# Optimization experiments

Measured on AMD Instinct MI355X. Metric: run time of the kernel, lower is better.

The kernel has to match this reference:

```python
import jax, jax.numpy as jnp
import numpy as np


def conv1x1(x, w, b):
    # x: [B,C,H,W], w: [O,C], b: [O]
    return jnp.einsum('oc,bchw->bohw', w, x) + b[None, :, None, None]


def interp_bilinear_ac(x, oh, ow):
    # bilinear resize with align_corners=True, x: [B,C,H,W] -> [B,C,oh,ow]
    B, C, H, W = x.shape
    if (H, W) == (oh, ow):
        return x
    ys = jnp.linspace(0.0, H - 1.0, oh)
    xs = jnp.linspace(0.0, W - 1.0, ow)
    y0 = jnp.clip(jnp.floor(ys).astype(jnp.int32), 0, H - 1)
    y1 = jnp.minimum(y0 + 1, H - 1)
    x0 = jnp.clip(jnp.floor(xs).astype(jnp.int32), 0, W - 1)
    x1 = jnp.minimum(x0 + 1, W - 1)
    wy = (ys - y0).astype(x.dtype)
    wx = (xs - x0).astype(x.dtype)
    top = x[:, :, y0, :] * (1 - wy)[None, None, :, None] + x[:, :, y1, :] * wy[None, None, :, None]
    out = top[:, :, :, x0] * (1 - wx)[None, None, None, :] + top[:, :, :, x1] * wx[None, None, None, :]
    return out


def non_local(x, qw, qb, kw, kb, vw, vb, ow_, ob):
    B, C, H, W = x.shape
    HW = H * W
    q = conv1x1(x, qw, qb).reshape(B, -1, HW)  # [B, Ci, HW]
    k = conv1x1(x, kw, kb).reshape(B, -1, HW)
    v = conv1x1(x, vw, vb).reshape(B, -1, HW)
    attn = jnp.einsum('bci,bcj->bij', q, k)     # [B, HW, HW]
    attn = jax.nn.softmax(attn, axis=-1)
    out = jnp.einsum('bcj,bij->bci', v, attn)   # [B, Ci, HW]
    out = out.reshape(B, -1, H, W)
    return conv1x1(out, ow_, ob)


def _forward(x1, x2, x3, x4, qw, qb, kw, kb, vw, vb, ow_, ob, g1w, g1b, g2w, g2b):
    H1, W1 = x1.shape[2], x1.shape[3]
    x2_up = interp_bilinear_ac(x2, H1, W1)
    x3_up = interp_bilinear_ac(x3, H1, W1)
    x4_up = interp_bilinear_ac(x4, H1, W1)
    gf = jnp.concatenate([x1, x2_up, x3_up, x4_up], axis=1)  # [B, 128, H1, W1]
    gf = non_local(gf, qw, qb, kw, kb, vw, vb, ow_, ob)
    h = jax.nn.relu(conv1x1(gf, g1w, g1b))
    sw = jax.nn.sigmoid(conv1x1(h, g2w, g2b))                # [B, 128, H1, W1]
    w1, w2, w3, w4 = sw[:, :32], sw[:, 32:64], sw[:, 64:96], sw[:, 96:128]
    x1_out = x1 * (1 + w1)
    x2_out = x2 * (1 + interp_bilinear_ac(w2, x2.shape[2], x2.shape[3]))
    x3_out = x3 * (1 + interp_bilinear_ac(w3, x3.shape[2], x3.shape[3]))
    x4_out = x4 * (1 + interp_bilinear_ac(w4, x4.shape[2], x4.shape[3]))
    return (x1_out, x2_out, x3_out, x4_out)


def setup_inputs() -> dict:
    key = jax.random.key(0)
    ks = jax.random.split(key, 16)
    C = 128  # channel*4
    Ci = 64  # inter_channel
    Cg = 32
    d = {
        'x1': jax.random.normal(ks[0], (8, 32, 64, 64), jnp.float32),
        'x2': jax.random.normal(ks[1], (8, 32, 32, 32), jnp.float32),
        'x3': jax.random.normal(ks[2], (8, 32, 16, 16), jnp.float32),
        'x4': jax.random.normal(ks[3], (8, 32, 8, 8), jnp.float32),
        'qw': jax.random.normal(ks[4], (Ci, C), jnp.float32) * 0.05,
        'qb': jnp.zeros((Ci,), jnp.float32),
        'kw': jax.random.normal(ks[5], (Ci, C), jnp.float32) * 0.05,
        'kb': jnp.zeros((Ci,), jnp.float32),
        'vw': jax.random.normal(ks[6], (Ci, C), jnp.float32) * 0.05,
        'vb': jnp.zeros((Ci,), jnp.float32),
        'ow_': jax.random.normal(ks[7], (C, Ci), jnp.float32) * 0.05,
        'ob': jnp.zeros((C,), jnp.float32),
        'g1w': jax.random.normal(ks[8], (Cg, C), jnp.float32) * 0.05,
        'g1b': jnp.zeros((Cg,), jnp.float32),
        'g2w': jax.random.normal(ks[9], (C, Cg), jnp.float32) * 0.05,
        'g2b': jnp.zeros((C,), jnp.float32),
    }
    return d


def reference(x1, x2, x3, x4, qw, qb, kw, kb, vw, vb, ow_, ob, g1w, g1b, g2w, g2b):
    return _forward(x1, x2, x3, x4, qw, qb, kw, kb, vw, vb, ow_, ob, g1w, g1b, g2w, g2b)
```

## Files before the change

### kernel.cpp

```cpp
#include <hip/hip_runtime.h>
#include <hip/hip_bf16.h>


typedef __attribute__((ext_vector_type(8))) short s16x8;
typedef __attribute__((ext_vector_type(4))) float f32x4;
typedef __attribute__((ext_vector_type(16))) float f32x16;

#define LOG2E 1.44269504088896340736f

__device__ __forceinline__ unsigned int f2bf(float f) {
    unsigned int u = __float_as_uint(f);
    u += 0x7fffu + ((u >> 16) & 1u);
    return u >> 16;
}
__device__ __forceinline__ unsigned int pk2bf(float a, float b) {
    union { __hip_bfloat162 h; unsigned int u; } cv;
    cv.h = __float22bfloat162_rn(make_float2(a, b));
    return cv.u;
}
__device__ __forceinline__ float bf2f(unsigned short u) {
    return __uint_as_float((unsigned int)u << 16);
}
__device__ __forceinline__ float fexp2(float x) { return __builtin_amdgcn_exp2f(x); }
__device__ __forceinline__ float frcp(float x)  { return __builtin_amdgcn_rcpf(x); }

__global__ __launch_bounds__(256) void k_prep(
    const float* __restrict__ qw, const float* __restrict__ qb,
    const float* __restrict__ kw, const float* __restrict__ kb,
    const float* __restrict__ vw, const float* __restrict__ vb,
    const float* __restrict__ ow, const float* __restrict__ g1w,
    const float* __restrict__ g2w,
    unsigned short* __restrict__ WTb, float* __restrict__ bqkv,
    unsigned short* __restrict__ owb, unsigned short* __restrict__ g1wb,
    unsigned short* __restrict__ g2wb) {
  int t = blockIdx.x * 256 + threadIdx.x;
  if (t < 192 * 128) {
    int oc = t >> 7, c = t & 127;
    float v;
    if (oc < 64)       v = qw[oc * 128 + c] * LOG2E;
    else if (oc < 128) v = kw[(oc - 64) * 128 + c];
    else               v = vw[(oc - 128) * 128 + c];
    WTb[t] = (unsigned short)f2bf(v);
  }
  if (t < 192) {
    float v;
    if (t < 64)       v = qb[t] * LOG2E;
    else if (t < 128) v = kb[t - 64];
    else              v = vb[t - 128];
    bqkv[t] = v;
  }
  if (t < 128 * 64) owb[t]  = (unsigned short)f2bf(ow[t]);
  if (t < 32 * 128) g1wb[t] = (unsigned short)f2bf(g1w[t]);
  if (t < 128 * 32) g2wb[t] = (unsigned short)f2bf(g2w[t]);
}

__global__ __launch_bounds__(256, 4) void k_qkv(
    const float* __restrict__ x1, const float* __restrict__ x2,
    const float* __restrict__ x3, const float* __restrict__ x4,
    const unsigned short* __restrict__ WTb, const float* __restrict__ bqkv,
    unsigned short* __restrict__ Qg, unsigned short* __restrict__ Kg,
    unsigned short* __restrict__ Vg) {
  __shared__ __align__(16) unsigned short gfb[32 * 136];
  unsigned int* gfbu = (unsigned int*)gfb;

  const int blk = blockIdx.x;
  const int b = blk >> 7;
  const int i0 = (blk & 127) << 5;
  const int t = threadIdx.x;
  const int wv = t >> 6, lane = t & 63;
  const int r = lane & 15, qd = lane >> 4;
  f32x4 zf = {0.f, 0.f, 0.f, 0.f};

  {
    const int cp = t >> 2, q = t & 3;
    const int c0 = cp << 1;
    const int pbase = q << 3;
    const int oy = i0 >> 6;
    const int ox0 = (i0 & 63) | (q << 3);

    if (cp < 16) {
      const float* s0 = x1 + (((b * 32 + c0) << 12) + (oy << 6) + ox0);
      const float* s1 = s0 + 4096;
      #pragma unroll
      for (int k4 = 0; k4 < 2; k4++) {
        float4 va = ((const float4*)s0)[k4];
        float4 vb = ((const float4*)s1)[k4];
        int p = pbase + k4 * 4;
        gfbu[(p + 0) * 68 + cp] = pk2bf(va.x, vb.x);
        gfbu[(p + 1) * 68 + cp] = pk2bf(va.y, vb.y);
        gfbu[(p + 2) * 68 + cp] = pk2bf(va.z, vb.z);
        gfbu[(p + 3) * 68 + cp] = pk2bf(va.w, vb.w);
      }
    } else {
      const float* base; int S, cs;
      if (cp < 32)      { base = x2; S = 32; cs = c0 - 32; }
      else if (cp < 48) { base = x3; S = 16; cs = c0 - 64; }
      else              { base = x4; S = 8;  cs = c0 - 96; }
      const float* pl0 = base + (b * 32 + cs) * S * S;
      const float* pl1 = pl0 + S * S;
      float yf = (float)oy * (float)(S - 1) * (1.0f / 63.0f);
      int y0 = (int)yf; if (y0 > S - 1) y0 = S - 1;
      int y1 = y0 + 1;  if (y1 > S - 1) y1 = S - 1;
      float wy = yf - (float)y0;
      const float* r00 = pl0 + y0 * S; const float* r01 = pl0 + y1 * S;
      const float* r10 = pl1 + y0 * S; const float* r11 = pl1 + y1 * S;
      for (int k = 0; k < 8; k++) {
        int ox = ox0 + k;
        float xf = (float)ox * (float)(S - 1) * (1.0f / 63.0f);
        int xx0 = (int)xf; if (xx0 > S - 1) xx0 = S - 1;
        int xx1 = xx0 + 1; if (xx1 > S - 1) xx1 = S - 1;
        float wx = xf - (float)xx0;
        float a0 = r00[xx0] + wx * (r00[xx1] - r00[xx0]);
        float b0 = r01[xx0] + wx * (r01[xx1] - r01[xx0]);
        float v0 = a0 + wy * (b0 - a0);
        float a1 = r10[xx0] + wx * (r10[xx1] - r10[xx0]);
        float b1 = r11[xx0] + wx * (r11[xx1] - r11[xx0]);
        float v1 = a1 + wy * (b1 - a1);
        gfbu[(pbase + k) * 68 + cp] = pk2bf(v0, v1);
      }
    }
  }
  __syncthreads();

  const int ocb = wv * 48;
  s16x8 af[3][4];
  float4 bias[3];
  #pragma unroll
  for (int mti = 0; mti < 3; mti++) {
    #pragma unroll
    for (int ks = 0; ks < 4; ks++)
      af[mti][ks] = *(const s16x8*)&WTb[(ocb + mti * 16 + r) * 128 + ks * 32 + qd * 8];
    bias[mti] = *(const float4*)&bqkv[ocb + mti * 16 + qd * 4];
  }

  #pragma unroll
  for (int nt = 0; nt < 2; nt++) {
    s16x8 bfr[4];
    #pragma unroll
    for (int ks = 0; ks < 4; ks++)
      bfr[ks] = *(const s16x8*)&gfb[(nt * 16 + r) * 136 + ks * 32 + qd * 8];
    f32x4 acc[3] = {zf, zf, zf};
    #pragma unroll
    for (int ks = 0; ks < 4; ks++)
      #pragma unroll
      for (int mti = 0; mti < 3; mti++)
        acc[mti] = __builtin_amdgcn_mfma_f32_16x16x32_bf16(af[mti][ks], bfr[ks], acc[mti], 0, 0, 0);

    const int pos = i0 + nt * 16 + r;
    #pragma unroll
    for (int mti = 0; mti < 3; mti++) {
      const int gmt = wv * 3 + mti;
      float ax = acc[mti].x + bias[mti].x;
      float ay = acc[mti].y + bias[mti].y;
      float az = acc[mti].z + bias[mti].z;
      float aw = acc[mti].w + bias[mti].w;
      if (gmt < 4) {
        uint2 w; w.x = pk2bf(ax, ay); w.y = pk2bf(az, aw);
        *(uint2*)&Qg[(((b << 12) + pos) << 6) + gmt * 16 + qd * 4] = w;
      } else if (gmt < 8) {
        uint2 w; w.x = pk2bf(ax, ay); w.y = pk2bf(az, aw);
        *(uint2*)&Kg[(((b << 12) + pos) << 6) + (gmt - 4) * 16 + qd * 4] = w;
      } else {
        int ocv = (gmt - 8) * 16 + qd * 4;
        Vg[((b * 64 + ocv + 0) << 12) + pos] = (unsigned short)f2bf(ax);
        Vg[((b * 64 + ocv + 1) << 12) + pos] = (unsigned short)f2bf(ay);
        Vg[((b * 64 + ocv + 2) << 12) + pos] = (unsigned short)f2bf(az);
        Vg[((b * 64 + ocv + 3) << 12) + pos] = (unsigned short)f2bf(aw);
      }
    }
  }
}

__global__ __launch_bounds__(256, 4) void k_attn(
    const unsigned short* __restrict__ Qg, const unsigned short* __restrict__ Kg,
    const unsigned short* __restrict__ Vg, unsigned short* __restrict__ Op,
    float* __restrict__ Lp) {
  __shared__ __align__(16) unsigned short Kl[2][64 * 72];
  __shared__ __align__(16) unsigned short Vl[2][64 * 72];

  const int b = blockIdx.x >> 7;
  const int part = (blockIdx.x >> 5) & 3;
  const int qg = blockIdx.x & 31;
  const int i0 = qg << 7;
  const int t = threadIdx.x;
  const int wv = t >> 6, lane = t & 63;
  const int q = lane & 31, hi = lane >> 5;
  const int qbase = i0 + wv * 32;

  s16x8 qf[4];
  #pragma unroll
  for (int kc = 0; kc < 4; kc++)
    qf[kc] = *(const s16x8*)&Qg[(((b << 12) + qbase + q) << 6) + kc * 16 + hi * 8];

  f32x16 acc[2];
  #pragma unroll
  for (int m = 0; m < 2; m++)
    #pragma unroll
    for (int e = 0; e < 16; e++) acc[m][e] = 0.f;
  float ls = 0.f;

  const int srow = t >> 3, sseg = t & 7;
  const unsigned short* kt0 = &Kg[(((b << 12) + (part << 10) + srow) << 6) + sseg * 8];
  const unsigned short* vt0 = &Vg[((b * 64 + srow) << 12) + (part << 10) + sseg * 8];
  uint4 pk0 = *(const uint4*)(kt0);
  uint4 pk1 = *(const uint4*)(kt0 + (32 << 6));
  uint4 pv0 = *(const uint4*)(vt0);
  uint4 pv1 = *(const uint4*)(vt0 + (32 << 12));

  for (int it = 0; it < 16; it++) {
    unsigned short* Kb = Kl[it & 1];
    unsigned short* Vb = Vl[it & 1];
    *(uint4*)&Kb[srow * 72 + sseg * 8] = pk0;
    *(uint4*)&Kb[(srow + 32) * 72 + sseg * 8] = pk1;
    *(uint4*)&Vb[srow * 72 + sseg * 8] = pv0;
    *(uint4*)&Vb[(srow + 32) * 72 + sseg * 8] = pv1;
    __syncthreads();
    if (it < 15) {
      int j0 = (it + 1) << 6;
      pk0 = *(const uint4*)(kt0 + (j0 << 6));
      pk1 = *(const uint4*)(kt0 + ((j0 + 32) << 6));
      pv0 = *(const uint4*)(vt0 + j0);
      pv1 = *(const uint4*)(vt0 + (32 << 12) + j0);
    }

    unsigned int pu[2][8];
    #pragma unroll
    for (int kt = 0; kt < 2; kt++) {
      f32x16 st;
      #pragma unroll
      for (int e = 0; e < 16; e++) st[e] = 0.f;
      #pragma unroll
      for (int kc = 0; kc < 4; kc++) {
        s16x8 kf = *(const s16x8*)&Kb[(kt * 32 + q) * 72 + kc * 16 + hi * 8];
        st = __builtin_amdgcn_mfma_f32_32x32x16_bf16(kf, qf[kc], st, 0, 0, 0);
      }
      float lsum = 0.f;
      #pragma unroll
      for (int i2 = 0; i2 < 8; i2++) {
        float p0 = fexp2(st[2 * i2]);
        float p1 = fexp2(st[2 * i2 + 1]);
        lsum += p0 + p1;
        pu[kt][i2] = pk2bf(p0, p1);
      }
      ls += lsum;
    }

    #pragma unroll
    for (int kt = 0; kt < 2; kt++) {
      #pragma unroll
      for (int c16 = 0; c16 < 2; c16++) {
        const int c16g = kt * 2 + c16;
        unsigned int a0 = pu[kt][c16 * 4 + 0], a1 = pu[kt][c16 * 4 + 1];
        unsigned int a2 = pu[kt][c16 * 4 + 2], a3 = pu[kt][c16 * 4 + 3];
        unsigned int k0 = hi ? a2 : a0, k1 = hi ? a3 : a1;
        unsigned int s0 = hi ? a0 : a2, s1 = hi ? a1 : a3;
        unsigned int r0 = __shfl_xor(s0, 32);
        unsigned int r1 = __shfl_xor(s1, 32);
        union { s16x8 v; unsigned int u[4]; } pb;
        pb.u[0] = hi ? r0 : k0;
        pb.u[1] = hi ? r1 : k1;
        pb.u[2] = hi ? k0 : r0;
        pb.u[3] = hi ? k1 : r1;
        #pragma unroll
        for (int mtv = 0; mtv < 2; mtv++) {
          s16x8 vf = *(const s16x8*)&Vb[(mtv * 32 + q) * 72 + c16g * 16 + hi * 8];
          acc[mtv] = __builtin_amdgcn_mfma_f32_32x32x16_bf16(vf, pb.v, acc[mtv], 0, 0, 0);
        }
      }
    }
  }

  ls += __shfl_xor(ls, 32);
  float inv = frcp(ls);
  const int qrow = qbase + q;
  unsigned short* orow = &Op[(((part * 8 + b) << 12) + qrow) << 6];
  #pragma unroll
  for (int mtv = 0; mtv < 2; mtv++) {
    #pragma unroll
    for (int i2 = 0; i2 < 8; i2++) {
      int dbase = ((2 * i2) & 3) + 8 * ((2 * i2) >> 2) + 4 * hi + mtv * 32;
      *(unsigned int*)&orow[dbase] =
          pk2bf(acc[mtv][2 * i2] * inv, acc[mtv][2 * i2 + 1] * inv);
    }
  }
  if (hi == 0) Lp[((part * 8 + b) << 12) + qrow] = ls;
}

__global__ __launch_bounds__(256, 4) void k_out(
    const unsigned short* __restrict__ Op, const float* __restrict__ Lp,
    const unsigned short* __restrict__ owb, const float* __restrict__ obias,
    const unsigned short* __restrict__ g1wb, const float* __restrict__ g1b,
    const unsigned short* __restrict__ g2wb, const float* __restrict__ g2b,
    const float* __restrict__ x1, float* __restrict__ out,
    unsigned short* __restrict__ SWb) {
  __shared__ __align__(16) unsigned short Ot[32 * 72];
  __shared__ __align__(16) unsigned short gf2t[32 * 136];
  __shared__ __align__(16) unsigned short ht[32 * 40];
  const int blk = blockIdx.x;
  const int b = blk >> 7;
  const int i0 = (blk & 127) << 5;
  const int t = threadIdx.x;
  const int wv = t >> 6, lane = t & 63;
  const int r = lane & 15, qd = lane >> 4;
  f32x4 zf = {0.f, 0.f, 0.f, 0.f};

  {
    const int pos = t >> 3, seg = t & 7;
    const int i = i0 + pos;
    float lp4[4], lsum = 0.f;
    #pragma unroll
    for (int p = 0; p < 4; p++) { lp4[p] = Lp[((p * 8 + b) << 12) + i]; lsum += lp4[p]; }
    float o[8];
    #pragma unroll
    for (int k = 0; k < 8; k++) o[k] = 0.f;
    float invs = frcp(lsum);
    #pragma unroll
    for (int p = 0; p < 4; p++) {
      float w = lp4[p] * invs;
      uint4 u = *(const uint4*)&Op[((((p * 8 + b) << 12) + i) << 6) + seg * 8];
      o[0] += w * __uint_as_float(u.x << 16);
      o[1] += w * __uint_as_float(u.x & 0xFFFF0000u);
      o[2] += w * __uint_as_float(u.y << 16);
      o[3] += w * __uint_as_float(u.y & 0xFFFF0000u);
      o[4] += w * __uint_as_float(u.z << 16);
      o[5] += w * __uint_as_float(u.z & 0xFFFF0000u);
      o[6] += w * __uint_as_float(u.w << 16);
      o[7] += w * __uint_as_float(u.w & 0xFFFF0000u);
    }
    unsigned int* dst = (unsigned int*)&Ot[pos * 72 + seg * 8];
    #pragma unroll
    for (int k = 0; k < 4; k++) dst[k] = pk2bf(o[2 * k], o[2 * k + 1]);
  }
  __syncthreads();

  {
    const int ocb = wv * 32;
    s16x8 af[2][2];
    #pragma unroll
    for (int mt = 0; mt < 2; mt++)
      #pragma unroll
      for (int ks = 0; ks < 2; ks++)
        af[mt][ks] = *(const s16x8*)&owb[(ocb + mt * 16 + r) * 64 + ks * 32 + qd * 8];
    float4 bias[2];
    #pragma unroll
    for (int mt = 0; mt < 2; mt++)
      bias[mt] = *(const float4*)&obias[ocb + mt * 16 + qd * 4];
    #pragma unroll
    for (int nt = 0; nt < 2; nt++) {
      s16x8 bfr[2];
      #pragma unroll
      for (int ks = 0; ks < 2; ks++)
        bfr[ks] = *(const s16x8*)&Ot[(nt * 16 + r) * 72 + ks * 32 + qd * 8];
      f32x4 acc[2] = {zf, zf};
      #pragma unroll
      for (int ks = 0; ks < 2; ks++)
        #pragma unroll
        for (int mt = 0; mt < 2; mt++)
          acc[mt] = __builtin_amdgcn_mfma_f32_16x16x32_bf16(af[mt][ks], bfr[ks], acc[mt], 0, 0, 0);
      #pragma unroll
      for (int mt = 0; mt < 2; mt++) {
        uint2 w;
        w.x = pk2bf(acc[mt].x + bias[mt].x, acc[mt].y + bias[mt].y);
        w.y = pk2bf(acc[mt].z + bias[mt].z, acc[mt].w + bias[mt].w);
        *(uint2*)&gf2t[(nt * 16 + r) * 136 + ocb + mt * 16 + qd * 4] = w;
      }
    }
  }
  __syncthreads();

  {
    const int mt = wv & 1, pt = wv >> 1;
    s16x8 af[4];
    #pragma unroll
    for (int ks = 0; ks < 4; ks++)
      af[ks] = *(const s16x8*)&g1wb[(mt * 16 + r) * 128 + ks * 32 + qd * 8];
    float4 bias = *(const float4*)&g1b[mt * 16 + qd * 4];
    s16x8 bfr[4];
    #pragma unroll
    for (int ks = 0; ks < 4; ks++)
      bfr[ks] = *(const s16x8*)&gf2t[(pt * 16 + r) * 136 + ks * 32 + qd * 8];
    f32x4 acc = zf;
    #pragma unroll
    for (int ks = 0; ks < 4; ks++)
      acc = __builtin_amdgcn_mfma_f32_16x16x32_bf16(af[ks], bfr[ks], acc, 0, 0, 0);
    uint2 w;
    w.x = pk2bf(fmaxf(acc.x + bias.x, 0.f), fmaxf(acc.y + bias.y, 0.f));
    w.y = pk2bf(fmaxf(acc.z + bias.z, 0.f), fmaxf(acc.w + bias.w, 0.f));
    *(uint2*)&ht[(pt * 16 + r) * 40 + mt * 16 + qd * 4] = w;
  }
  __syncthreads();

  {
    const int nb = wv * 32;
    s16x8 bfg[2];
    float bias[2];
    #pragma unroll
    for (int ntl = 0; ntl < 2; ntl++) {
      bfg[ntl] = *(const s16x8*)&g2wb[(nb + ntl * 16 + r) * 32 + qd * 8];
      bias[ntl] = g2b[nb + ntl * 16 + r];
    }
    #pragma unroll
    for (int mt = 0; mt < 2; mt++) {
      s16x8 af = *(const s16x8*)&ht[(mt * 16 + r) * 40 + qd * 8];
      #pragma unroll
      for (int ntl = 0; ntl < 2; ntl++) {
        f32x4 acc = __builtin_amdgcn_mfma_f32_16x16x32_bf16(af, bfg[ntl], zf, 0, 0, 0);
        const int oc3 = nb + ntl * 16 + r;
        float s0 = frcp(1.0f + fexp2(-LOG2E * (acc.x + bias[ntl])));
        float s1 = frcp(1.0f + fexp2(-LOG2E * (acc.y + bias[ntl])));
        float s2 = frcp(1.0f + fexp2(-LOG2E * (acc.z + bias[ntl])));
        float s3 = frcp(1.0f + fexp2(-LOG2E * (acc.w + bias[ntl])));
        if (nb == 0) {
          const int off = ((b * 32 + oc3) << 12) + i0 + mt * 16 + qd * 4;
          float4 xv = *(const float4*)&x1[off];
          float4 o4;
          o4.x = xv.x * (1.f + s0); o4.y = xv.y * (1.f + s1);
          o4.z = xv.z * (1.f + s2); o4.w = xv.w * (1.f + s3);
          *(float4*)&out[off] = o4;
        } else {
          uint2 w; w.x = pk2bf(s0, s1); w.y = pk2bf(s2, s3);
          *(uint2*)&SWb[((b * 128 + oc3) << 12) + i0 + mt * 16 + qd * 4] = w;
        }
      }
    }
  }
}

__device__ __forceinline__ float bilin64(const unsigned short* __restrict__ p,
                                         int oy, int ox, int n) {
  float yf = (float)oy * 63.0f / (float)n;
  int y0 = (int)yf; if (y0 > 63) y0 = 63;
  int y1 = y0 + 1;  if (y1 > 63) y1 = 63;
  float wy = yf - (float)y0;
  float xf = (float)ox * 63.0f / (float)n;
  int x0 = (int)xf; if (x0 > 63) x0 = 63;
  int x1 = x0 + 1;  if (x1 > 63) x1 = 63;
  float wx = xf - (float)x0;
  float v00 = bf2f(p[y0 * 64 + x0]), v01 = bf2f(p[y0 * 64 + x1]);
  float v10 = bf2f(p[y1 * 64 + x0]), v11 = bf2f(p[y1 * 64 + x1]);
  float top = v00 + wx * (v01 - v00);
  float bot = v10 + wx * (v11 - v10);
  return top + wy * (bot - top);
}

__global__ __launch_bounds__(256) void k_final(
    const float* __restrict__ x2, const float* __restrict__ x3,
    const float* __restrict__ x4,
    const unsigned short* __restrict__ SWb, float* __restrict__ out) {
  const int N1 = 1048576, N2 = 262144, N3 = 65536, N4 = 16384;
  int idx = blockIdx.x * 256 + threadIdx.x;
  if (idx < N2) {
    int b = idx >> 15, rr = idx & 32767;
    int c = rr >> 10, oy = (rr >> 5) & 31, ox = rr & 31;
    float w = bilin64(SWb + ((b * 128 + 32 + c) << 12), oy, ox, 31);
    out[N1 + idx] = x2[idx] * (1.f + w);
  } else if (idx < N2 + N3) {
    int i3 = idx - N2;
    int b = i3 >> 13, rr = i3 & 8191;
    int c = rr >> 8, oy = (rr >> 4) & 15, ox = rr & 15;
    float w = bilin64(SWb + ((b * 128 + 64 + c) << 12), oy, ox, 15);
    out[N1 + idx] = x3[i3] * (1.f + w);
  } else if (idx < N2 + N3 + N4) {
    int i4 = idx - N2 - N3;
    int b = i4 >> 11, rr = i4 & 2047;
    int c = rr >> 6, oy = (rr >> 3) & 7, ox = rr & 7;
    float w = bilin64(SWb + ((b * 128 + 96 + c) << 12), oy, ox, 7);
    out[N1 + idx] = x4[i4] * (1.f + w);
  }
}

extern "C" void kernel_launch(void* const* d_in, const int* in_sizes, int n_in,
                              void* d_out, int out_size, void* d_ws, size_t ws_size,
                              hipStream_t stream) {
  const float* x1  = (const float*)d_in[0];
  const float* x2  = (const float*)d_in[1];
  const float* x3  = (const float*)d_in[2];
  const float* x4  = (const float*)d_in[3];
  const float* qw  = (const float*)d_in[4];
  const float* qb  = (const float*)d_in[5];
  const float* kw  = (const float*)d_in[6];
  const float* kb  = (const float*)d_in[7];
  const float* vw  = (const float*)d_in[8];
  const float* vb  = (const float*)d_in[9];
  const float* ow  = (const float*)d_in[10];
  const float* ob  = (const float*)d_in[11];
  const float* g1w = (const float*)d_in[12];
  const float* g1b = (const float*)d_in[13];
  const float* g2w = (const float*)d_in[14];
  const float* g2b = (const float*)d_in[15];
  float* out = (float*)d_out;

  char* ws = (char*)d_ws;
  unsigned short* Qg  = (unsigned short*)(ws + 0);
  unsigned short* Kg  = (unsigned short*)(ws + 4194304);
  unsigned short* Vg  = (unsigned short*)(ws + 8388608);
  unsigned short* SWb = (unsigned short*)(ws + 0);
  unsigned short* Op  = (unsigned short*)(ws + 12582912);
  float* Lp   = (float*)(ws + 29360128);
  unsigned short* WTb = (unsigned short*)(ws + 29884416);
  float* bqkv = (float*)(ws + 29933568);
  unsigned short* owb  = (unsigned short*)(ws + 29934592);
  unsigned short* g1wb = (unsigned short*)(ws + 29950976);
  unsigned short* g2wb = (unsigned short*)(ws + 29959168);

  k_prep<<<96, 256, 0, stream>>>(qw, qb, kw, kb, vw, vb, ow, g1w, g2w,
                                 WTb, bqkv, owb, g1wb, g2wb);
  k_qkv<<<1024, 256, 0, stream>>>(x1, x2, x3, x4, WTb, bqkv, Qg, Kg, Vg);
  k_attn<<<1024, 256, 0, stream>>>(Qg, Kg, Vg, Op, Lp);
  k_out<<<1024, 256, 0, stream>>>(Op, Lp, owb, ob, g1wb, g1b, g2wb, g2b,
                                  x1, out, SWb);
  k_final<<<1344, 256, 0, stream>>>(x2, x3, x4, SWb, out);
}
```

Measured before the change: 173.8 us.

## Fuse output projection, gating and final resize into attention via atomic counters

Merges k_out and k_final into k_attn. The last of the four key-partition blocks for each query group, detected with an atomic counter, merges the partial results and runs the output conv and gating MLP. The last of those blocks per batch then does the bilinear resize and the final multiply. This removes two kernel launches and their inter-kernel gaps. In exchange, the tail work is serialized onto a few blocks, with one block per batch doing all the x2/x3/x4 output work, and a memset is added to reset the counters.

```diff
diff --git a/kernel.cpp b/kernel.cpp
--- a/kernel.cpp
+++ b/kernel.cpp
@@ -174,9 +174,17 @@
 __global__ __launch_bounds__(256, 4) void k_attn(
     const unsigned short* __restrict__ Qg, const unsigned short* __restrict__ Kg,
     const unsigned short* __restrict__ Vg, unsigned short* __restrict__ Op,
-    float* __restrict__ Lp) {
+    float* __restrict__ Lp,
+    const unsigned short* __restrict__ owb, const float* __restrict__ obias,
+    const unsigned short* __restrict__ g1wb, const float* __restrict__ g1b,
+    const unsigned short* __restrict__ g2wb, const float* __restrict__ g2b,
+    const float* __restrict__ x1, const float* __restrict__ x2,
+    const float* __restrict__ x3, const float* __restrict__ x4,
+    float* __restrict__ out, unsigned short* __restrict__ SWb2,
+    unsigned int* __restrict__ cnt1, unsigned int* __restrict__ cnt2) {
   __shared__ __align__(16) unsigned short Kl[2][64 * 72];
   __shared__ __align__(16) unsigned short Vl[2][64 * 72];
+  __shared__ unsigned int whoS;
 
   const int b = blockIdx.x >> 7;
   const int part = (blockIdx.x >> 5) & 3;
@@ -187,285 +195,313 @@
   const int q = lane & 31, hi = lane >> 5;
   const int qbase = i0 + wv * 32;
 
-  s16x8 qf[4];
-  #pragma unroll
-  for (int kc = 0; kc < 4; kc++)
-    qf[kc] = *(const s16x8*)&Qg[(((b << 12) + qbase + q) << 6) + kc * 16 + hi * 8];
-
-  f32x16 acc[2];
-  #pragma unroll
-  for (int m = 0; m < 2; m++)
-    #pragma unroll
-    for (int e = 0; e < 16; e++) acc[m][e] = 0.f;
-  float ls = 0.f;
-
-  const int srow = t >> 3, sseg = t & 7;
-  const unsigned short* kt0 = &Kg[(((b << 12) + (part << 10) + srow) << 6) + sseg * 8];
-  const unsigned short* vt0 = &Vg[((b * 64 + srow) << 12) + (part << 10) + sseg * 8];
-  uint4 pk0 = *(const uint4*)(kt0);
-  uint4 pk1 = *(const uint4*)(kt0 + (32 << 6));
-  uint4 pv0 = *(const uint4*)(vt0);
-  uint4 pv1 = *(const uint4*)(vt0 + (32 << 12));
-
-  for (int it = 0; it < 16; it++) {
-    unsigned short* Kb = Kl[it & 1];
-    unsigned short* Vb = Vl[it & 1];
-    *(uint4*)&Kb[srow * 72 + sseg * 8] = pk0;
-    *(uint4*)&Kb[(srow + 32) * 72 + sseg * 8] = pk1;
-    *(uint4*)&Vb[srow * 72 + sseg * 8] = pv0;
-    *(uint4*)&Vb[(srow + 32) * 72 + sseg * 8] = pv1;
-    __syncthreads();
-    if (it < 15) {
-      int j0 = (it + 1) << 6;
-      pk0 = *(const uint4*)(kt0 + (j0 << 6));
-      pk1 = *(const uint4*)(kt0 + ((j0 + 32) << 6));
-      pv0 = *(const uint4*)(vt0 + j0);
-      pv1 = *(const uint4*)(vt0 + (32 << 12) + j0);
-    }
-
-    unsigned int pu[2][8];
-    #pragma unroll
-    for (int kt = 0; kt < 2; kt++) {
-      f32x16 st;
-      #pragma unroll
-      for (int e = 0; e < 16; e++) st[e] = 0.f;
-      #pragma unroll
-      for (int kc = 0; kc < 4; kc++) {
-        s16x8 kf = *(const s16x8*)&Kb[(kt * 32 + q) * 72 + kc * 16 + hi * 8];
-        st = __builtin_amdgcn_mfma_f32_32x32x16_bf16(kf, qf[kc], st, 0, 0, 0);
-      }
-      float lsum = 0.f;
+  {
+    s16x8 qf[4];
+    #pragma unroll
+    for (int kc = 0; kc < 4; kc++)
+      qf[kc] = *(const s16x8*)&Qg[(((b << 12) + qbase + q) << 6) + kc * 16 + hi * 8];
+
+    f32x16 acc[2];
+    #pragma unroll
+    for (int m = 0; m < 2; m++)
+      #pragma unroll
+      for (int e = 0; e < 16; e++) acc[m][e] = 0.f;
+    float ls = 0.f;
+
+    const int srow = t >> 3, sseg = t & 7;
+    const unsigned short* kt0 = &Kg[(((b << 12) + (part << 10) + srow) << 6) + sseg * 8];
+    const unsigned short* vt0 = &Vg[((b * 64 + srow) << 12) + (part << 10) + sseg * 8];
+    uint4 pk0 = *(const uint4*)(kt0);
+    uint4 pk1 = *(const uint4*)(kt0 + (32 << 6));
+    uint4 pv0 = *(const uint4*)(vt0);
+    uint4 pv1 = *(const uint4*)(vt0 + (32 << 12));
+
+    for (int it = 0; it < 16; it++) {
+      unsigned short* Kb = Kl[it & 1];
+      unsigned short* Vb = Vl[it & 1];
+      *(uint4*)&Kb[srow * 72 + sseg * 8] = pk0;
+      *(uint4*)&Kb[(srow + 32) * 72 + sseg * 8] = pk1;
+      *(uint4*)&Vb[srow * 72 + sseg * 8] = pv0;
+      *(uint4*)&Vb[(srow + 32) * 72 + sseg * 8] = pv1;
+      __syncthreads();
+      if (it < 15) {
+        int j0 = (it + 1) << 6;
+        pk0 = *(const uint4*)(kt0 + (j0 << 6));
+        pk1 = *(const uint4*)(kt0 + ((j0 + 32) << 6));
+        pv0 = *(const uint4*)(vt0 + j0);
+        pv1 = *(const uint4*)(vt0 + (32 << 12) + j0);
+      }
+
+      unsigned int pu[2][8];
+      #pragma unroll
+      for (int kt = 0; kt < 2; kt++) {
+        f32x16 st;
+        #pragma unroll
+        for (int e = 0; e < 16; e++) st[e] = 0.f;
+        #pragma unroll
+        for (int kc = 0; kc < 4; kc++) {
+          s16x8 kf = *(const s16x8*)&Kb[(kt * 32 + q) * 72 + kc * 16 + hi * 8];
+          st = __builtin_amdgcn_mfma_f32_32x32x16_bf16(kf, qf[kc], st, 0, 0, 0);
+        }
+        float lsum = 0.f;
+        #pragma unroll
+        for (int i2 = 0; i2 < 8; i2++) {
+          float p0 = fexp2(st[2 * i2]);
+          float p1 = fexp2(st[2 * i2 + 1]);
+          lsum += p0 + p1;
+          pu[kt][i2] = pk2bf(p0, p1);
+        }
+        ls += lsum;
+      }
+
+      #pragma unroll
+      for (int kt = 0; kt < 2; kt++) {
+        #pragma unroll
+        for (int c16 = 0; c16 < 2; c16++) {
+          const int c16g = kt * 2 + c16;
+          unsigned int a0 = pu[kt][c16 * 4 + 0], a1 = pu[kt][c16 * 4 + 1];
+          unsigned int a2 = pu[kt][c16 * 4 + 2], a3 = pu[kt][c16 * 4 + 3];
+          unsigned int k0 = hi ? a2 : a0, k1 = hi ? a3 : a1;
+          unsigned int s0 = hi ? a0 : a2, s1 = hi ? a1 : a3;
+          unsigned int r0 = __shfl_xor(s0, 32);
+          unsigned int r1 = __shfl_xor(s1, 32);
+          union { s16x8 v; unsigned int u[4]; } pb;
+          pb.u[0] = hi ? r0 : k0;
+          pb.u[1] = hi ? r1 : k1;
+          pb.u[2] = hi ? k0 : r0;
+          pb.u[3] = hi ? k1 : r1;
+          #pragma unroll
+          for (int mtv = 0; mtv < 2; mtv++) {
+            s16x8 vf = *(const s16x8*)&Vl[it & 1][(mtv * 32 + q) * 72 + c16g * 16 + hi * 8];
+            acc[mtv] = __builtin_amdgcn_mfma_f32_32x32x16_bf16(vf, pb.v, acc[mtv], 0, 0, 0);
+          }
+        }
+      }
+    }
+
+    ls += __shfl_xor(ls, 32);
+    float inv = frcp(ls);
+    const int qrow = qbase + q;
+    unsigned short* orow = &Op[(((part * 8 + b) << 12) + qrow) << 6];
+    #pragma unroll
+    for (int mtv = 0; mtv < 2; mtv++) {
       #pragma unroll
       for (int i2 = 0; i2 < 8; i2++) {
-        float p0 = fexp2(st[2 * i2]);
-        float p1 = fexp2(st[2 * i2 + 1]);
-        lsum += p0 + p1;
-        pu[kt][i2] = pk2bf(p0, p1);
-      }
-      ls += lsum;
-    }
-
-    #pragma unroll
-    for (int kt = 0; kt < 2; kt++) {
-      #pragma unroll
-      for (int c16 = 0; c16 < 2; c16++) {
-        const int c16g = kt * 2 + c16;
-        unsigned int a0 = pu[kt][c16 * 4 + 0], a1 = pu[kt][c16 * 4 + 1];
-        unsigned int a2 = pu[kt][c16 * 4 + 2], a3 = pu[kt][c16 * 4 + 3];
-        unsigned int k0 = hi ? a2 : a0, k1 = hi ? a3 : a1;
-        unsigned int s0 = hi ? a0 : a2, s1 = hi ? a1 : a3;
-        unsigned int r0 = __shfl_xor(s0, 32);
-        unsigned int r1 = __shfl_xor(s1, 32);
-        union { s16x8 v; unsigned int u[4]; } pb;
-        pb.u[0] = hi ? r0 : k0;
-        pb.u[1] = hi ? r1 : k1;
-        pb.u[2] = hi ? k0 : r0;
-        pb.u[3] = hi ? k1 : r1;
-        #pragma unroll
-        for (int mtv = 0; mtv < 2; mtv++) {
-          s16x8 vf = *(const s16x8*)&Vb[(mtv * 32 + q) * 72 + c16g * 16 + hi * 8];
-          acc[mtv] = __builtin_amdgcn_mfma_f32_32x32x16_bf16(vf, pb.v, acc[mtv], 0, 0, 0);
-        }
-      }
-    }
-  }
-
-  ls += __shfl_xor(ls, 32);
-  float inv = frcp(ls);
-  const int qrow = qbase + q;
-  unsigned short* orow = &Op[(((part * 8 + b) << 12) + qrow) << 6];
-  #pragma unroll
-  for (int mtv = 0; mtv < 2; mtv++) {
-    #pragma unroll
-    for (int i2 = 0; i2 < 8; i2++) {
-      int dbase = ((2 * i2) & 3) + 8 * ((2 * i2) >> 2) + 4 * hi + mtv * 32;
-      *(unsigned int*)&orow[dbase] =
-          pk2bf(acc[mtv][2 * i2] * inv, acc[mtv][2 * i2 + 1] * inv);
-    }
-  }
-  if (hi == 0) Lp[((part * 8 + b) << 12) + qrow] = ls;
-}
-
-__global__ __launch_bounds__(256, 4) void k_out(
-    const unsigned short* __restrict__ Op, const float* __restrict__ Lp,
-    const unsigned short* __restrict__ owb, const float* __restrict__ obias,
-    const unsigned short* __restrict__ g1wb, const float* __restrict__ g1b,
-    const unsigned short* __restrict__ g2wb, const float* __restrict__ g2b,
-    const float* __restrict__ x1, float* __restrict__ out,
-    unsigned short* __restrict__ SWb) {
-  __shared__ __align__(16) unsigned short Ot[32 * 72];
-  __shared__ __align__(16) unsigned short gf2t[32 * 136];
-  __shared__ __align__(16) unsigned short ht[32 * 40];
-  const int blk = blockIdx.x;
-  const int b = blk >> 7;
-  const int i0 = (blk & 127) << 5;
-  const int t = threadIdx.x;
-  const int wv = t >> 6, lane = t & 63;
+        int dbase = ((2 * i2) & 3) + 8 * ((2 * i2) >> 2) + 4 * hi + mtv * 32;
+        *(unsigned int*)&orow[dbase] =
+            pk2bf(acc[mtv][2 * i2] * inv, acc[mtv][2 * i2 + 1] * inv);
+      }
+    }
+    if (hi == 0) Lp[((part * 8 + b) << 12) + qrow] = ls;
+  }
+
+  __threadfence();
+  __syncthreads();
+  if (t == 0) whoS = atomicAdd(&cnt1[(b << 5) + qg], 1u);
+  __syncthreads();
+  if (whoS != 3) return;
+  __threadfence();
+
+  unsigned short* Ot   = &Kl[0][0];
+  unsigned short* gf2t = Ot + 2304;
+  unsigned short* ht   = gf2t + 4352;
   const int r = lane & 15, qd = lane >> 4;
   f32x4 zf = {0.f, 0.f, 0.f, 0.f};
 
+  for (int sub = 0; sub < 4; sub++) {
+    const int i0c = i0 + sub * 32;
+    __syncthreads();
+
+    {
+      const int pos = t >> 3, seg = t & 7;
+      const int i = i0c + pos;
+      float lp4[4], lsum = 0.f;
+      #pragma unroll
+      for (int p = 0; p < 4; p++) { lp4[p] = Lp[((p * 8 + b) << 12) + i]; lsum += lp4[p]; }
+      float o[8];
+      #pragma unroll
+      for (int k = 0; k < 8; k++) o[k] = 0.f;
+      float invs = frcp(lsum);
+      #pragma unroll
+      for (int p = 0; p < 4; p++) {
+        float w = lp4[p] * invs;
+        uint4 u = *(const uint4*)&Op[((((p * 8 + b) << 12) + i) << 6) + seg * 8];
+        o[0] += w * __uint_as_float(u.x << 16);
+        o[1] += w * __uint_as_float(u.x & 0xFFFF0000u);
+        o[2] += w * __uint_as_float(u.y << 16);
+        o[3] += w * __uint_as_float(u.y & 0xFFFF0000u);
+        o[4] += w * __uint_as_float(u.z << 16);
+        o[5] += w * __uint_as_float(u.z & 0xFFFF0000u);
+        o[6] += w * __uint_as_float(u.w << 16);
+        o[7] += w * __uint_as_float(u.w & 0xFFFF0000u);
+      }
+      unsigned int* dst = (unsigned int*)&Ot[pos * 72 + seg * 8];
+      #pragma unroll
+      for (int k = 0; k < 4; k++) dst[k] = pk2bf(o[2 * k], o[2 * k + 1]);
+    }
+    __syncthreads();
+
+    {
+      const int ocb = wv * 32;
+      s16x8 af[2][2];
+      #pragma unroll
+      for (int mt = 0; mt < 2; mt++)
+        #pragma unroll
+        for (int ks = 0; ks < 2; ks++)
+          af[mt][ks] = *(const s16x8*)&owb[(ocb + mt * 16 + r) * 64 + ks * 32 + qd * 8];
+      float4 bias[2];
+      #pragma unroll
+      for (int mt = 0; mt < 2; mt++)
+        bias[mt] = *(const float4*)&obias[ocb + mt * 16 + qd * 4];
+      #pragma unroll
+      for (int nt = 0; nt < 2; nt++) {
+        s16x8 bfr[2];
+        #pragma unroll
+        for (int ks = 0; ks < 2; ks++)
+          bfr[ks] = *(const s16x8*)&Ot[(nt * 16 + r) * 72 + ks * 32 + qd * 8];
+        f32x4 acc2[2] = {zf, zf};
+        #pragma unroll
+        for (int ks = 0; ks < 2; ks++)
+          #pragma unroll
+          for (int mt = 0; mt < 2; mt++)
+            acc2[mt] = __builtin_amdgcn_mfma_f32_16x16x32_bf16(af[mt][ks], bfr[ks], acc2[mt], 0, 0, 0);
+        #pragma unroll
+        for (int mt = 0; mt < 2; mt++) {
+          uint2 w;
+          w.x = pk2bf(acc2[mt].x + bias[mt].x, acc2[mt].y + bias[mt].y);
+          w.y = pk2bf(acc2[mt].z + bias[mt].z, acc2[mt].w + bias[mt].w);
+          *(uint2*)&gf2t[(nt * 16 + r) * 136 + ocb + mt * 16 + qd * 4] = w;
+        }
+      }
+    }
+    __syncthreads();
+
+    {
+      const int mt = wv & 1, pt = wv >> 1;
+      s16x8 af[4];
+      #pragma unroll
+      for (int ks = 0; ks < 4; ks++)
+        af[ks] = *(const s16x8*)&g1wb[(mt * 16 + r) * 128 + ks * 32 + qd * 8];
+      float4 bias = *(const float4*)&g1b[mt * 16 + qd * 4];
+      s16x8 bfr[4];
+      #pragma unroll
+      for (int ks = 0; ks < 4; ks++)
+        bfr[ks] = *(const s16x8*)&gf2t[(pt * 16 + r) * 136 + ks * 32 + qd * 8];
+      f32x4 acc2 = zf;
+      #pragma unroll
+      for (int ks = 0; ks < 4; ks++)
+        acc2 = __builtin_amdgcn_mfma_f32_16x16x32_bf16(af[ks], bfr[ks], acc2, 0, 0, 0);
+      uint2 w;
+      w.x = pk2bf(fmaxf(acc2.x + bias.x, 0.f), fmaxf(acc2.y + bias.y, 0.f));
+      w.y = pk2bf(fmaxf(acc2.z + bias.z, 0.f), fmaxf(acc2.w + bias.w, 0.f));
+      *(uint2*)&ht[(pt * 16 + r) * 40 + mt * 16 + qd * 4] = w;
+    }
+    __syncthreads();
+
+    {
+      const int nb = wv * 32;
+      s16x8 bfg[2];
+      float bias[2];
+      #pragma unroll
+      for (int ntl = 0; ntl < 2; ntl++) {
+        bfg[ntl] = *(const s16x8*)&g2wb[(nb + ntl * 16 + r) * 32 + qd * 8];
+        bias[ntl] = g2b[nb + ntl * 16 + r];
+      }
+      #pragma unroll
+      for (int mt = 0; mt < 2; mt++) {
+        s16x8 af = *(const s16x8*)&ht[(mt * 16 + r) * 40 + qd * 8];
+        #pragma unroll
+        for (int ntl = 0; ntl < 2; ntl++) {
+          f32x4 acc2 = __builtin_amdgcn_mfma_f32_16x16x32_bf16(af, bfg[ntl], zf, 0, 0, 0);
+          const int oc3 = nb + ntl * 16 + r;
+          float s0 = frcp(1.0f + fexp2(-LOG2E * (acc2.x + bias[ntl])));
+          float s1 = frcp(1.0f + fexp2(-LOG2E * (acc2.y + bias[ntl])));
+          float s2 = frcp(1.0f + fexp2(-LOG2E * (acc2.z + bias[ntl])));
+          float s3 = frcp(1.0f + fexp2(-LOG2E * (acc2.w + bias[ntl])));
+          if (nb == 0) {
+            const int off = ((b * 32 + oc3) << 12) + i0c + mt * 16 + qd * 4;
+            float4 xv = *(const float4*)&x1[off];
+            float4 o4;
+            o4.x = xv.x * (1.f + s0); o4.y = xv.y * (1.f + s1);
+            o4.z = xv.z * (1.f + s2); o4.w = xv.w * (1.f + s3);
+            *(float4*)&out[off] = o4;
+          } else {
+            uint2 w; w.x = pk2bf(s0, s1); w.y = pk2bf(s2, s3);
+            *(uint2*)&SWb2[((b * 96 + (oc3 - 32)) << 12) + i0c + mt * 16 + qd * 4] = w;
+          }
+        }
+      }
+    }
+  }
+
+  __threadfence();
+  __syncthreads();
+  if (t == 0) whoS = atomicAdd(&cnt2[b], 1u);
+  __syncthreads();
+  if (whoS != 31) return;
+  __threadfence();
+
   {
-    const int pos = t >> 3, seg = t & 7;
-    const int i = i0 + pos;
-    float lp4[4], lsum = 0.f;
-    #pragma unroll
-    for (int p = 0; p < 4; p++) { lp4[p] = Lp[((p * 8 + b) << 12) + i]; lsum += lp4[p]; }
-    float o[8];
-    #pragma unroll
-    for (int k = 0; k < 8; k++) o[k] = 0.f;
-    float invs = frcp(lsum);
-    #pragma unroll
-    for (int p = 0; p < 4; p++) {
-      float w = lp4[p] * invs;
-      uint4 u = *(const uint4*)&Op[((((p * 8 + b) << 12) + i) << 6) + seg * 8];
-      o[0] += w * __uint_as_float(u.x << 16);
-      o[1] += w * __uint_as_float(u.x & 0xFFFF0000u);
-      o[2] += w * __uint_as_float(u.y << 16);
-      o[3] += w * __uint_as_float(u.y & 0xFFFF0000u);
-      o[4] += w * __uint_as_float(u.z << 16);
-      o[5] += w * __uint_as_float(u.z & 0xFFFF0000u);
-      o[6] += w * __uint_as_float(u.w << 16);
-      o[7] += w * __uint_as_float(u.w & 0xFFFF0000u);
-    }
-    unsigned int* dst = (unsigned int*)&Ot[pos * 72 + seg * 8];
-    #pragma unroll
-    for (int k = 0; k < 4; k++) dst[k] = pk2bf(o[2 * k], o[2 * k + 1]);
-  }
-  __syncthreads();
-
-  {
-    const int ocb = wv * 32;
-    s16x8 af[2][2];
-    #pragma unroll
-    for (int mt = 0; mt < 2; mt++)
-      #pragma unroll
-      for (int ks = 0; ks < 2; ks++)
-        af[mt][ks] = *(const s16x8*)&owb[(ocb + mt * 16 + r) * 64 + ks * 32 + qd * 8];
-    float4 bias[2];
-    #pragma unroll
-    for (int mt = 0; mt < 2; mt++)
-      bias[mt] = *(const float4*)&obias[ocb + mt * 16 + qd * 4];
-    #pragma unroll
-    for (int nt = 0; nt < 2; nt++) {
-      s16x8 bfr[2];
-      #pragma unroll
-      for (int ks = 0; ks < 2; ks++)
-        bfr[ks] = *(const s16x8*)&Ot[(nt * 16 + r) * 72 + ks * 32 + qd * 8];
-      f32x4 acc[2] = {zf, zf};
-      #pragma unroll
-      for (int ks = 0; ks < 2; ks++)
-        #pragma unroll
-        for (int mt = 0; mt < 2; mt++)
-          acc[mt] = __builtin_amdgcn_mfma_f32_16x16x32_bf16(af[mt][ks], bfr[ks], acc[mt], 0, 0, 0);
-      #pragma unroll
-      for (int mt = 0; mt < 2; mt++) {
-        uint2 w;
-        w.x = pk2bf(acc[mt].x + bias[mt].x, acc[mt].y + bias[mt].y);
-        w.y = pk2bf(acc[mt].z + bias[mt].z, acc[mt].w + bias[mt].w);
-        *(uint2*)&gf2t[(nt * 16 + r) * 136 + ocb + mt * 16 + qd * 4] = w;
-      }
-    }
-  }
-  __syncthreads();
-
-  {
-    const int mt = wv & 1, pt = wv >> 1;
-    s16x8 af[4];
-    #pragma unroll
-    for (int ks = 0; ks < 4; ks++)
-      af[ks] = *(const s16x8*)&g1wb[(mt * 16 + r) * 128 + ks * 32 + qd * 8];
-    float4 bias = *(const float4*)&g1b[mt * 16 + qd * 4];
-    s16x8 bfr[4];
-    #pragma unroll
-    for (int ks = 0; ks < 4; ks++)
-      bfr[ks] = *(const s16x8*)&gf2t[(pt * 16 + r) * 136 + ks * 32 + qd * 8];
-    f32x4 acc = zf;
-    #pragma unroll
-    for (int ks = 0; ks < 4; ks++)
-      acc = __builtin_amdgcn_mfma_f32_16x16x32_bf16(af[ks], bfr[ks], acc, 0, 0, 0);
-    uint2 w;
-    w.x = pk2bf(fmaxf(acc.x + bias.x, 0.f), fmaxf(acc.y + bias.y, 0.f));
-    w.y = pk2bf(fmaxf(acc.z + bias.z, 0.f), fmaxf(acc.w + bias.w, 0.f));
-    *(uint2*)&ht[(pt * 16 + r) * 40 + mt * 16 + qd * 4] = w;
-  }
-  __syncthreads();
-
-  {
-    const int nb = wv * 32;
-    s16x8 bfg[2];
-    float bias[2];
-    #pragma unroll
-    for (int ntl = 0; ntl < 2; ntl++) {
-      bfg[ntl] = *(const s16x8*)&g2wb[(nb + ntl * 16 + r) * 32 + qd * 8];
-      bias[ntl] = g2b[nb + ntl * 16 + r];
-    }
-    #pragma unroll
-    for (int mt = 0; mt < 2; mt++) {
-      s16x8 af = *(const s16x8*)&ht[(mt * 16 + r) * 40 + qd * 8];
-      #pragma unroll
-      for (int ntl = 0; ntl < 2; ntl++) {
-        f32x4 acc = __builtin_amdgcn_mfma_f32_16x16x32_bf16(af, bfg[ntl], zf, 0, 0, 0);
-        const int oc3 = nb + ntl * 16 + r;
-        float s0 = frcp(1.0f + fexp2(-LOG2E * (acc.x + bias[ntl])));
-        float s1 = frcp(1.0f + fexp2(-LOG2E * (acc.y + bias[ntl])));
-        float s2 = frcp(1.0f + fexp2(-LOG2E * (acc.z + bias[ntl])));
-        float s3 = frcp(1.0f + fexp2(-LOG2E * (acc.w + bias[ntl])));
-        if (nb == 0) {
-          const int off = ((b * 32 + oc3) << 12) + i0 + mt * 16 + qd * 4;
-          float4 xv = *(const float4*)&x1[off];
-          float4 o4;
-          o4.x = xv.x * (1.f + s0); o4.y = xv.y * (1.f + s1);
-          o4.z = xv.z * (1.f + s2); o4.w = xv.w * (1.f + s3);
-          *(float4*)&out[off] = o4;
-        } else {
-          uint2 w; w.x = pk2bf(s0, s1); w.y = pk2bf(s2, s3);
-          *(uint2*)&SWb[((b * 128 + oc3) << 12) + i0 + mt * 16 + qd * 4] = w;
-        }
-      }
-    }
-  }
-}
-
-__device__ __forceinline__ float bilin64(const unsigned short* __restrict__ p,
-                                         int oy, int ox, int n) {
-  float yf = (float)oy * 63.0f / (float)n;
-  int y0 = (int)yf; if (y0 > 63) y0 = 63;
-  int y1 = y0 + 1;  if (y1 > 63) y1 = 63;
-  float wy = yf - (float)y0;
-  float xf = (float)ox * 63.0f / (float)n;
-  int x0 = (int)xf; if (x0 > 63) x0 = 63;
-  int x1 = x0 + 1;  if (x1 > 63) x1 = 63;
-  float wx = xf - (float)x0;
-  float v00 = bf2f(p[y0 * 64 + x0]), v01 = bf2f(p[y0 * 64 + x1]);
-  float v10 = bf2f(p[y1 * 64 + x0]), v11 = bf2f(p[y1 * 64 + x1]);
-  float top = v00 + wx * (v01 - v00);
-  float bot = v10 + wx * (v11 - v10);
-  return top + wy * (bot - top);
-}
-
-__global__ __launch_bounds__(256) void k_final(
-    const float* __restrict__ x2, const float* __restrict__ x3,
-    const float* __restrict__ x4,
-    const unsigned short* __restrict__ SWb, float* __restrict__ out) {
-  const int N1 = 1048576, N2 = 262144, N3 = 65536, N4 = 16384;
-  int idx = blockIdx.x * 256 + threadIdx.x;
-  if (idx < N2) {
-    int b = idx >> 15, rr = idx & 32767;
-    int c = rr >> 10, oy = (rr >> 5) & 31, ox = rr & 31;
-    float w = bilin64(SWb + ((b * 128 + 32 + c) << 12), oy, ox, 31);
-    out[N1 + idx] = x2[idx] * (1.f + w);
-  } else if (idx < N2 + N3) {
-    int i3 = idx - N2;
-    int b = i3 >> 13, rr = i3 & 8191;
-    int c = rr >> 8, oy = (rr >> 4) & 15, ox = rr & 15;
-    float w = bilin64(SWb + ((b * 128 + 64 + c) << 12), oy, ox, 15);
-    out[N1 + idx] = x3[i3] * (1.f + w);
-  } else if (idx < N2 + N3 + N4) {
-    int i4 = idx - N2 - N3;
-    int b = i4 >> 11, rr = i4 & 2047;
-    int c = rr >> 6, oy = (rr >> 3) & 7, ox = rr & 7;
-    float w = bilin64(SWb + ((b * 128 + 96 + c) << 12), oy, ox, 7);
-    out[N1 + idx] = x4[i4] * (1.f + w);
+    const int N1 = 1048576;
+    for (int idx = t; idx < 43008; idx += 256) {
+      if (idx < 32768) {
+        int c = idx >> 10, oy = (idx >> 5) & 31, ox = idx & 31;
+        const unsigned short* p = SWb2 + ((b * 96 + c) << 12);
+        float yf = (float)oy * 63.0f / 31.0f;
+        int y0 = (int)yf; if (y0 > 63) y0 = 63;
+        int y1 = y0 + 1;  if (y1 > 63) y1 = 63;
+        float wy = yf - (float)y0;
+        float xf = (float)ox * 63.0f / 31.0f;
+        int x0 = (int)xf; if (x0 > 63) x0 = 63;
+        int xx1 = x0 + 1; if (xx1 > 63) xx1 = 63;
+        float wx = xf - (float)x0;
+        float v00 = bf2f(p[y0 * 64 + x0]), v01 = bf2f(p[y0 * 64 + xx1]);
+        float v10 = bf2f(p[y1 * 64 + x0]), v11 = bf2f(p[y1 * 64 + xx1]);
+        float top = v00 + wx * (v01 - v00);
+        float bot = v10 + wx * (v11 - v10);
+        float w = top + wy * (bot - top);
+        int gi = b * 32768 + idx;
+        out[N1 + gi] = x2[gi] * (1.f + w);
+      } else if (idx < 40960) {
+        int j = idx - 32768;
+        int c = j >> 8, oy = (j >> 4) & 15, ox = j & 15;
+        const unsigned short* p = SWb2 + ((b * 96 + 32 + c) << 12);
+        float yf = (float)oy * 63.0f / 15.0f;
+        int y0 = (int)yf; if (y0 > 63) y0 = 63;
+        int y1 = y0 + 1;  if (y1 > 63) y1 = 63;
+        float wy = yf - (float)y0;
+        float xf = (float)ox * 63.0f / 15.0f;
+        int x0 = (int)xf; if (x0 > 63) x0 = 63;
+        int xx1 = x0 + 1; if (xx1 > 63) xx1 = 63;
+        float wx = xf - (float)x0;
+        float v00 = bf2f(p[y0 * 64 + x0]), v01 = bf2f(p[y0 * 64 + xx1]);
+        float v10 = bf2f(p[y1 * 64 + x0]), v11 = bf2f(p[y1 * 64 + xx1]);
+        float top = v00 + wx * (v01 - v00);
+        float bot = v10 + wx * (v11 - v10);
+        float w = top + wy * (bot - top);
+        int gi = b * 8192 + j;
+        out[N1 + 262144 + gi] = x3[gi] * (1.f + w);
+      } else {
+        int j = idx - 40960;
+        int c = j >> 6, oy = (j >> 3) & 7, ox = j & 7;
+        const unsigned short* p = SWb2 + ((b * 96 + 64 + c) << 12);
+        float yf = (float)oy * 63.0f / 7.0f;
+        int y0 = (int)yf; if (y0 > 63) y0 = 63;
+        int y1 = y0 + 1;  if (y1 > 63) y1 = 63;
+        float wy = yf - (float)y0;
+        float xf = (float)ox * 63.0f / 7.0f;
+        int x0 = (int)xf; if (x0 > 63) x0 = 63;
+        int xx1 = x0 + 1; if (xx1 > 63) xx1 = 63;
+        float wx = xf - (float)x0;
+        float v00 = bf2f(p[y0 * 64 + x0]), v01 = bf2f(p[y0 * 64 + xx1]);
+        float v10 = bf2f(p[y1 * 64 + x0]), v11 = bf2f(p[y1 * 64 + xx1]);
+        float top = v00 + wx * (v01 - v00);
+        float bot = v10 + wx * (v11 - v10);
+        float w = top + wy * (bot - top);
+        int gi = b * 2048 + j;
+        out[N1 + 262144 + 65536 + gi] = x4[gi] * (1.f + w);
+      }
+    }
   }
 }
 
@@ -494,7 +530,6 @@
   unsigned short* Qg  = (unsigned short*)(ws + 0);
   unsigned short* Kg  = (unsigned short*)(ws + 4194304);
   unsigned short* Vg  = (unsigned short*)(ws + 8388608);
-  unsigned short* SWb = (unsigned short*)(ws + 0);
   unsigned short* Op  = (unsigned short*)(ws + 12582912);
   float* Lp   = (float*)(ws + 29360128);
   unsigned short* WTb = (unsigned short*)(ws + 29884416);
@@ -502,12 +537,15 @@
   unsigned short* owb  = (unsigned short*)(ws + 29934592);
   unsigned short* g1wb = (unsigned short*)(ws + 29950976);
   unsigned short* g2wb = (unsigned short*)(ws + 29959168);
-
+  unsigned int* cnt1 = (unsigned int*)(ws + 29967360);
+  unsigned int* cnt2 = (unsigned int*)(ws + 29968384);
+  unsigned short* SWb2 = (unsigned short*)(ws + 29969408);
+
+  hipMemsetAsync(ws + 29967360, 0, 2048, stream);
   k_prep<<<96, 256, 0, stream>>>(qw, qb, kw, kb, vw, vb, ow, g1w, g2w,
                                  WTb, bqkv, owb, g1wb, g2wb);
   k_qkv<<<1024, 256, 0, stream>>>(x1, x2, x3, x4, WTb, bqkv, Qg, Kg, Vg);
-  k_attn<<<1024, 256, 0, stream>>>(Qg, Kg, Vg, Op, Lp);
-  k_out<<<1024, 256, 0, stream>>>(Op, Lp, owb, ob, g1wb, g1b, g2wb, g2b,
-                                  x1, out, SWb);
-  k_final<<<1344, 256, 0, stream>>>(x2, x3, x4, SWb, out);
-}
+  k_attn<<<1024, 256, 0, stream>>>(Qg, Kg, Vg, Op, Lp,
+                                   owb, ob, g1wb, g1b, g2wb, g2b,
+                                   x1, x2, x3, x4, out, SWb2, cnt1, cnt2);
+}
```

New measurement: 477.7 us. +174.9%, slower.
